# Kernel tuning notes

Measured on AMD Instinct MI355X. Metric: run time of the kernel, lower is better.

The kernel has to match this reference:

```python
import jax, jax.numpy as jnp
import numpy as np

N_STATE = 128      # HiPPO state size (hardcoded N=128 in module)
SEQ = 8192         # sequence length
D_HEAD = 16        # d_model=128 // n_head=8, used only for score scaling
OUT_DIM = 1000     # hardcoded self.out_dim
STEP = 1e-3        # step_size


def _legs_matrices(N):
    # HiPPO-LegS: A[n,k] = -sqrt(2n+1)sqrt(2k+1) (n>k), -(n+1) (n==k), 0 else; B[n]=sqrt(2n+1)
    n = np.arange(N, dtype=np.float64)
    pre = np.sqrt(2.0 * n + 1.0)
    A = -np.tril(pre[:, None] * pre[None, :], -1) - np.diag(n + 1.0)
    B = pre.copy()
    return A, B


def setup_inputs() -> dict:
    key = jax.random.key(0)
    kq, kk, kv, kw = jax.random.split(key, 4)
    A_np, B_np = _legs_matrices(N_STATE)
    A = jnp.asarray(A_np, jnp.float32)
    B = jnp.asarray(B_np, jnp.float32)
    # ZOH discretization (GBT_alpha=2.0 > 1 in repo => zero-order hold)
    GA = jax.scipy.linalg.expm(STEP * A)                       # (N, N)
    GB = jnp.linalg.solve(A, (GA - jnp.eye(N_STATE)) @ B)      # (N,)
    # xavier-uniform proj kernel (128 -> 1000), zero bias
    lim = float(np.sqrt(6.0 / (N_STATE + OUT_DIM)))
    Wp = jax.random.uniform(kw, (N_STATE, OUT_DIM), jnp.float32, -lim, lim)
    bp = jnp.zeros((OUT_DIM,), jnp.float32)
    return {
        "query": jax.random.normal(kq, (SEQ, 1), jnp.float32),
        "key": jax.random.normal(kk, (SEQ, 1), jnp.float32),
        "value": jax.random.normal(kv, (SEQ, 1), jnp.float32),
        "GA": GA,
        "GB": GB,
        "Wp": Wp,
        "bp": bp,
    }


def _hippo_scan(GA, GB, fs):
    # fs: (3, S) scalar input sequences; carry c: (3, N)
    def step(c, ft):
        c = c @ GA.T + ft[:, None] * GB[None, :]
        return c, c
    c0 = jnp.zeros((fs.shape[0], GA.shape[0]), GA.dtype)
    _, cs = jax.lax.scan(step, c0, fs.T)   # cs: (S, 3, N)
    return cs


def reference(query, key, value, GA, GB, Wp, bp):
    fs = jnp.stack([query[:, 0], key[:, 0], value[:, 0]])  # (3, S)
    cs = _hippo_scan(GA, GB, fs)                            # (S, 3, N)
    q, k, v = cs[:, 0, :], cs[:, 1, :], cs[:, 2, :]         # (S, N) each
    score = (q @ k.T) / jnp.sqrt(jnp.asarray(D_HEAD, q.dtype))  # (S, S)
    attn = jax.nn.softmax(score, axis=-1)
    context = attn @ v                                      # (S, N)
    out = context @ Wp + bp                                 # (S, OUT_DIM)
    return out, attn
```

## Files before the change

kernel.cpp:

```cpp
#include <hip/hip_runtime.h>

static constexpr int N  = 128;
static constexpr int S  = 8192;
static constexpr int L  = 128;
static constexpr int NC = 64;
static constexpr int OD = 1000;
static constexpr int KSPLIT = 16;
#define SCL 0.25f

typedef unsigned short u16;
typedef __attribute__((ext_vector_type(4))) unsigned short us4;
typedef __attribute__((ext_vector_type(8))) unsigned short us8;
typedef __attribute__((ext_vector_type(8))) short bf16x8;
typedef __attribute__((ext_vector_type(4))) float f32x4;

__device__ __forceinline__ u16 f2bf(float x){
  unsigned u = __float_as_uint(x);
  u += 0x7FFFu + ((u >> 16) & 1u);
  return (u16)(u >> 16);
}
__device__ __forceinline__ float bf2f(u16 h){
  return __uint_as_float(((unsigned)h) << 16);
}

__global__ void k_copyT(const float* __restrict__ GA, float* __restrict__ QT1){
  int idx = blockIdx.x*256 + threadIdx.x;
  int m = idx >> 7, n = idx & 127;
  QT1[idx] = GA[n*N + m];
}

__global__ __launch_bounds__(256) void k_powmm(float* QT, int mlev){
  int i = blockIdx.z + 1;
  const float* Am = QT + (size_t)mlev*(N*N);
  const float* Ai = QT + (size_t)i*(N*N);
  float* C = QT + (size_t)(mlev+i)*(N*N);
  __shared__ __align__(16) float As[16][68];
  __shared__ __align__(16) float Bs[16][68];
  int bm = blockIdx.y, bn = blockIdx.x;
  int tx = threadIdx.x, ty = threadIdx.y;
  int tid = ty*16 + tx;
  float acc[4][4] = {};
  for (int kt = 0; kt < N; kt += 16){
    int row = tid >> 2, kc = (tid & 3) << 2;
    float4 av = *(const float4*)(Am + (size_t)(bm*64+row)*N + kt + kc);
    As[kc+0][row]=av.x; As[kc+1][row]=av.y; As[kc+2][row]=av.z; As[kc+3][row]=av.w;
    int bk = tid >> 4, c0 = (tid & 15) << 2;
    *(float4*)&Bs[bk][c0] = *(const float4*)(Ai + (size_t)(kt+bk)*N + bn*64 + c0);
    __syncthreads();
#pragma unroll
    for (int kk = 0; kk < 16; ++kk){
      float4 a = *(const float4*)&As[kk][ty*4];
      float4 b = *(const float4*)&Bs[kk][tx*4];
      float aa[4]={a.x,a.y,a.z,a.w}, bb[4]={b.x,b.y,b.z,b.w};
#pragma unroll
      for (int ii=0; ii<4; ++ii)
#pragma unroll
        for (int jj=0; jj<4; ++jj) acc[ii][jj] += aa[ii]*bb[jj];
    }
    __syncthreads();
  }
#pragma unroll
  for (int ii=0; ii<4; ++ii){
    float4 vst = make_float4(acc[ii][0],acc[ii][1],acc[ii][2],acc[ii][3]);
    *(float4*)(C + (size_t)(bm*64+ty*4+ii)*N + bn*64 + tx*4) = vst;
  }
}

__global__ void k_g(const float* __restrict__ QT, const float* __restrict__ GB,
                    float* __restrict__ g){
  int kb = blockIdx.x;
  int n = threadIdx.x;
  if (kb == 0){ g[n] = GB[n]; return; }
  const float* Qk = QT + (size_t)kb*(N*N);
  float acc = 0.0f;
  for (int m = 0; m < N; ++m) acc += Qk[m*N + n]*GB[m];
  g[kb*N + n] = acc;
}

__global__ __launch_bounds__(256) void k_fill_local(const float* __restrict__ fq,
                             const float* __restrict__ fk, const float* __restrict__ fv,
                             const float* __restrict__ g, float* __restrict__ cs){
  int tile = blockIdx.x;
  int s = blockIdx.y, j = blockIdx.z;
  const float* f = (s==0)? fq : (s==1)? fk : fv;
  __shared__ float flp[256];
  __shared__ __align__(16) float Bs[16][68];
  int tx = threadIdx.x, ty = threadIdx.y;
  int tid = ty*16 + tx;
  flp[tid] = (tid < 128) ? 0.0f : f[j*L + tid - 128];
  int ti = tile >> 1, tj = tile & 1;
  float acc[4][4] = {};
  int kmax = (ti == 0) ? 64 : 128;
  for (int kt = 0; kt < kmax; kt += 16){
    int bk = tid >> 4, c0 = (tid & 15) << 2;
    *(float4*)&Bs[bk][c0] = *(const float4*)(g + (size_t)(kt+bk)*N + tj*64 + c0);
    __syncthreads();
#pragma unroll
    for (int kk = 0; kk < 16; ++kk){
      float4 b = *(const float4*)&Bs[kk][tx*4];
      int base = 128 + ti*64 + ty*4 - kt - kk;
      float aa[4] = {flp[base], flp[base+1], flp[base+2], flp[base+3]};
      float bb[4] = {b.x, b.y, b.z, b.w};
#pragma unroll
      for (int ii=0; ii<4; ++ii)
#pragma unroll
        for (int jj=0; jj<4; ++jj) acc[ii][jj] += aa[ii]*bb[jj];
    }
    __syncthreads();
  }
#pragma unroll
  for (int ii=0; ii<4; ++ii){
    int row = ti*64 + ty*4 + ii;
    float4 vst = make_float4(acc[ii][0],acc[ii][1],acc[ii][2],acc[ii][3]);
    *(float4*)(cs + ((size_t)s*S + (size_t)j*L + row)*N + tj*64 + tx*4) = vst;
  }
}

__global__ void k_bscan(const float* __restrict__ QT, const float* __restrict__ cs,
                        float* __restrict__ bounds){
  __shared__ float bc[3][N];
  __shared__ float bnx[3][N];
  int tid = threadIdx.x;
  int s = tid >> 7, n = tid & 127;
  const float* QL = QT + (size_t)L*(N*N);
  bc[s][n] = 0.0f;
  bounds[(0*3+s)*N + n] = 0.0f;
  __syncthreads();
  for (int j = 0; j < NC; ++j){
    float acc = cs[((size_t)s*S + (size_t)j*L + 127)*N + n];
    for (int m = 0; m < N; ++m) acc += QL[m*N+n]*bc[s][m];
    bnx[s][n] = acc;
    bounds[((j+1)*3+s)*N + n] = acc;
    __syncthreads();
    bc[s][n] = bnx[s][n];
    __syncthreads();
  }
}

__global__ __launch_bounds__(256) void k_fill_bound(const float* __restrict__ QT,
                          const float* __restrict__ bounds, float* __restrict__ cs){
  int i = blockIdx.x;
  int jg = blockIdx.y;
  __shared__ float Qs[N*N];
  int tid = threadIdx.x;
  int p = tid >> 7, n = tid & 127;
  const float* Qg = QT + (size_t)(i+1)*(N*N);
  for (int idx = tid; idx < N*N; idx += 256) Qs[idx] = Qg[idx];
  __syncthreads();
  for (int r4 = 0; r4 < 24; r4 += 4){
    int task0 = jg*48 + p*24 + r4;
    const float* b0 = bounds + (size_t)task0*N;
    const float* b1 = b0 + N;
    const float* b2 = b0 + 2*N;
    const float* b3 = b0 + 3*N;
    float a0=0.f, a1=0.f, a2=0.f, a3=0.f;
#pragma unroll 4
    for (int m = 0; m < N; ++m){
      float q = Qs[m*N + n];
      a0 += q*b0[m]; a1 += q*b1[m]; a2 += q*b2[m]; a3 += q*b3[m];
    }
    float av[4] = {a0, a1, a2, a3};
#pragma unroll
    for (int q4 = 0; q4 < 4; ++q4){
      int task = task0 + q4;
      int j = task/3, s2 = task - 3*j;
      cs[((size_t)s2*S + (size_t)j*L + i)*N + n] += av[q4];
    }
  }
}

__global__ void k_split_qk(const float* __restrict__ cs,
                           u16* __restrict__ sh, u16* __restrict__ sl){
  size_t i = ((size_t)blockIdx.x*256 + threadIdx.x) << 2;
  float4 v = *(const float4*)(cs + i);
  us4 h, l;
  h[0]=f2bf(v.x); l[0]=f2bf(v.x - bf2f(h[0]));
  h[1]=f2bf(v.y); l[1]=f2bf(v.y - bf2f(h[1]));
  h[2]=f2bf(v.z); l[2]=f2bf(v.z - bf2f(h[2]));
  h[3]=f2bf(v.w); l[3]=f2bf(v.w - bf2f(h[3]));
  *(us4*)(sh + i) = h;
  *(us4*)(sl + i) = l;
}

__global__ __launch_bounds__(256) void k_split_vT(const float* __restrict__ vs,
                           u16* __restrict__ vth, u16* __restrict__ vtl){
  __shared__ u16 Th[128*72];
  __shared__ u16 Tl[128*72];
  int t0 = blockIdx.x * 64;
  int tid = threadIdx.x;
  for (int c = tid; c < 2048; c += 256){
    int i = c >> 5, n0 = (c & 31) << 2;
    float4 v = *(const float4*)(vs + (size_t)(t0 + i)*N + n0);
    u16 h;
    h = f2bf(v.x); Th[(n0+0)*72 + i] = h; Tl[(n0+0)*72 + i] = f2bf(v.x - bf2f(h));
    h = f2bf(v.y); Th[(n0+1)*72 + i] = h; Tl[(n0+1)*72 + i] = f2bf(v.y - bf2f(h));
    h = f2bf(v.z); Th[(n0+2)*72 + i] = h; Tl[(n0+2)*72 + i] = f2bf(v.z - bf2f(h));
    h = f2bf(v.w); Th[(n0+3)*72 + i] = h; Tl[(n0+3)*72 + i] = f2bf(v.w - bf2f(h));
  }
  __syncthreads();
  for (int c = tid; c < 1024; c += 256){
    int n = c >> 3, tc = (c & 7) << 3;
    int tile = (t0 + tc) >> 5;
    int kin  = (t0 + tc) & 31;
    size_t dst = (size_t)tile*4096 + n*32 + kin;
    *(us8*)(vth + dst) = *(const us8*)&Th[n*72 + tc];
    *(us8*)(vtl + dst) = *(const us8*)&Tl[n*72 + tc];
  }
}

__global__ __launch_bounds__(256) void k_stats(
    const u16* __restrict__ qh, const u16* __restrict__ ql,
    const u16* __restrict__ kh, const u16* __restrict__ kl,
    float* __restrict__ pmax, float* __restrict__ psum){
  __shared__ __align__(16) u16 Ah[128*40], Al[128*40], Bh[128*40], Bl[128*40];
  __shared__ float wst[2][128][2];
  int bm = blockIdx.y, bn = blockIdx.x;
  int tid = threadIdx.x;
  int lane = tid & 63, w = tid >> 6;
  int l15 = lane & 15, l4 = lane >> 4;
  int wr = w >> 1, wc = w & 1;
  int kg = l4 << 3;
  f32x4 accs[4][4] = {};
  for (int kt = 0; kt < N; kt += 32){
    for (int c = tid; c < 512; c += 256){
      int r = c >> 2, k8 = (c & 3) << 3;
      size_t ga = (size_t)(bm*128 + r)*N + kt + k8;
      size_t gb = (size_t)(bn*128 + r)*N + kt + k8;
      int lo = r*40 + k8;
      *(us8*)&Ah[lo] = *(const us8*)(qh + ga);
      *(us8*)&Al[lo] = *(const us8*)(ql + ga);
      *(us8*)&Bh[lo] = *(const us8*)(kh + gb);
      *(us8*)&Bl[lo] = *(const us8*)(kl + gb);
    }
    __syncthreads();
    bf16x8 kfh[4], kfl[4], qfh[4], qfl[4];
#pragma unroll
    for (int si = 0; si < 4; ++si){
      kfh[si] = *(const bf16x8*)&Bh[(wr*64 + si*16 + l15)*40 + kg];
      kfl[si] = *(const bf16x8*)&Bl[(wr*64 + si*16 + l15)*40 + kg];
    }
#pragma unroll
    for (int qi = 0; qi < 4; ++qi){
      qfh[qi] = *(const bf16x8*)&Ah[(wc*64 + qi*16 + l15)*40 + kg];
      qfl[qi] = *(const bf16x8*)&Al[(wc*64 + qi*16 + l15)*40 + kg];
    }
#pragma unroll
    for (int si = 0; si < 4; ++si)
#pragma unroll
      for (int qi = 0; qi < 4; ++qi){
        accs[si][qi] = __builtin_amdgcn_mfma_f32_16x16x32_bf16(kfh[si], qfh[qi], accs[si][qi], 0,0,0);
        accs[si][qi] = __builtin_amdgcn_mfma_f32_16x16x32_bf16(kfh[si], qfl[qi], accs[si][qi], 0,0,0);
        accs[si][qi] = __builtin_amdgcn_mfma_f32_16x16x32_bf16(kfl[si], qfh[qi], accs[si][qi], 0,0,0);
      }
    __syncthreads();
  }
  float mq[4], sq[4];
#pragma unroll
  for (int qi = 0; qi < 4; ++qi){
    float m = -3.0e38f;
#pragma unroll
    for (int si = 0; si < 4; ++si)
#pragma unroll
      for (int r = 0; r < 4; ++r) m = fmaxf(m, accs[si][qi][r]);
    mq[qi] = m * SCL;
  }
#pragma unroll
  for (int qi = 0; qi < 4; ++qi){
    mq[qi] = fmaxf(mq[qi], __shfl_xor(mq[qi], 16, 64));
    mq[qi] = fmaxf(mq[qi], __shfl_xor(mq[qi], 32, 64));
  }
#pragma unroll
  for (int qi = 0; qi < 4; ++qi){
    float s = 0.0f;
#pragma unroll
    for (int si = 0; si < 4; ++si)
#pragma unroll
      for (int r = 0; r < 4; ++r) s += __expf(accs[si][qi][r]*SCL - mq[qi]);
    sq[qi] = s;
  }
#pragma unroll
  for (int qi = 0; qi < 4; ++qi){
    sq[qi] += __shfl_xor(sq[qi], 16, 64);
    sq[qi] += __shfl_xor(sq[qi], 32, 64);
  }
  if (l4 == 0){
#pragma unroll
    for (int qi = 0; qi < 4; ++qi){
      int ql_ = wc*64 + qi*16 + l15;
      wst[wr][ql_][0] = mq[qi];
      wst[wr][ql_][1] = sq[qi];
    }
  }
  __syncthreads();
  if (tid < 128){
    float m0 = wst[0][tid][0], m1 = wst[1][tid][0];
    float m = fmaxf(m0, m1);
    float Z = wst[0][tid][1]*__expf(m0 - m) + wst[1][tid][1]*__expf(m1 - m);
    pmax[(size_t)bn*S + bm*128 + tid] = m;
    psum[(size_t)bn*S + bm*128 + tid] = Z;
  }
}

__global__ void k_rowstat(const float* __restrict__ pmax, const float* __restrict__ psum,
                          float* __restrict__ rowm, float* __restrict__ rowinv){
  int t = blockIdx.x*256 + threadIdx.x;
  float m = -3.0e38f;
  for (int b = 0; b < 64; ++b) m = fmaxf(m, pmax[(size_t)b*S + t]);
  float Z = 0.0f;
  for (int b = 0; b < 64; ++b) Z += psum[(size_t)b*S + t]*__expf(pmax[(size_t)b*S + t] - m);
  rowm[t] = m;
  rowinv[t] = 1.0f/Z;
}

__global__ __launch_bounds__(256) void k_ctx(
    float* __restrict__ attn,
    const float* __restrict__ rowm, const float* __restrict__ rowinv,
    const u16* __restrict__ qh, const u16* __restrict__ ql,
    const u16* __restrict__ kh, const u16* __restrict__ kl,
    const u16* __restrict__ vth, const u16* __restrict__ vtl,
    float* __restrict__ dst, int mode){
  __shared__ __align__(16) u16 Ksh[32*136], Ksl[32*136];
  __shared__ __align__(16) u16 Vsh[128*40], Vsl[128*40];
  int bm = blockIdx.x, kz = blockIdx.y;
  int tid = threadIdx.x, lane = tid & 63, w = tid >> 6;
  int l15 = lane & 15, l4 = lane >> 4;
  int kg = l4 << 3;
  const int KC = S / KSPLIT;
  int k0 = kz*KC;
  int qrow0 = bm*128 + w*32;
  bf16x8 qfh[2][4], qfl[2][4];
  float rm[2], ri[2];
#pragma unroll
  for (int qi = 0; qi < 2; ++qi){
    int q = qrow0 + qi*16 + l15;
#pragma unroll
    for (int kt = 0; kt < 4; ++kt){
      qfh[qi][kt] = *(const bf16x8*)(qh + (size_t)q*N + kt*32 + kg);
      qfl[qi][kt] = *(const bf16x8*)(ql + (size_t)q*N + kt*32 + kg);
    }
    rm[qi] = rowm[q];
    ri[qi] = rowinv[q];
  }
  f32x4 acco[2][8] = {};
  for (int ko = 0; ko < KC/32; ++ko){
    int cb = k0 + ko*32;
    for (int c = tid; c < 512; c += 256){
      int rr = c >> 4, k8 = (c & 15) << 3;
      size_t gk = (size_t)(cb + rr)*N + k8;
      *(us8*)&Ksh[rr*136 + k8] = *(const us8*)(kh + gk);
      *(us8*)&Ksl[rr*136 + k8] = *(const us8*)(kl + gk);
    }
    {
      const u16* sh = vth + (size_t)(cb >> 5)*4096;
      const u16* sl = vtl + (size_t)(cb >> 5)*4096;
      for (int c = tid; c < 512; c += 256){
        int n = c >> 2, k8 = (c & 3) << 3;
        *(us8*)&Vsh[n*40 + k8] = *(const us8*)(sh + (size_t)c*8);
        *(us8*)&Vsl[n*40 + k8] = *(const us8*)(sl + (size_t)c*8);
      }
    }
    __syncthreads();
    f32x4 accs[2][2] = {};
#pragma unroll
    for (int kt = 0; kt < 4; ++kt){
      bf16x8 kfh[2], kfl[2];
#pragma unroll
      for (int si = 0; si < 2; ++si){
        kfh[si] = *(const bf16x8*)&Ksh[(si*16 + l15)*136 + kt*32 + kg];
        kfl[si] = *(const bf16x8*)&Ksl[(si*16 + l15)*136 + kt*32 + kg];
      }
#pragma unroll
      for (int si = 0; si < 2; ++si)
#pragma unroll
        for (int qi = 0; qi < 2; ++qi){
          accs[si][qi] = __builtin_amdgcn_mfma_f32_16x16x32_bf16(kfh[si], qfh[qi][kt], accs[si][qi], 0,0,0);
          accs[si][qi] = __builtin_amdgcn_mfma_f32_16x16x32_bf16(kfh[si], qfl[qi][kt], accs[si][qi], 0,0,0);
          accs[si][qi] = __builtin_amdgcn_mfma_f32_16x16x32_bf16(kfl[si], qfh[qi][kt], accs[si][qi], 0,0,0);
        }
    }
    bf16x8 pah[2][2], pal[2][2];
#pragma unroll
    for (int si = 0; si < 2; ++si)
#pragma unroll
      for (int qi = 0; qi < 2; ++qi){
        float p0 = __expf(accs[si][qi][0]*SCL - rm[qi]) * ri[qi];
        float p1 = __expf(accs[si][qi][1]*SCL - rm[qi]) * ri[qi];
        float p2 = __expf(accs[si][qi][2]*SCL - rm[qi]) * ri[qi];
        float p3 = __expf(accs[si][qi][3]*SCL - rm[qi]) * ri[qi];
        int q = qrow0 + qi*16 + l15;
        *(float4*)(attn + (size_t)q*S + cb + si*16 + (l4<<2)) = make_float4(p0,p1,p2,p3);
        u16 h0=f2bf(p0), h1=f2bf(p1), h2=f2bf(p2), h3=f2bf(p3);
        u16 e0=f2bf(p0-bf2f(h0)), e1=f2bf(p1-bf2f(h1)), e2=f2bf(p2-bf2f(h2)), e3=f2bf(p3-bf2f(h3));
        bf16x8 ah; ah[0]=(short)h0; ah[1]=(short)h1; ah[2]=(short)h2; ah[3]=(short)h3;
        ah[4]=0; ah[5]=0; ah[6]=0; ah[7]=0;
        bf16x8 al; al[0]=(short)e0; al[1]=(short)e1; al[2]=(short)e2; al[3]=(short)e3;
        al[4]=0; al[5]=0; al[6]=0; al[7]=0;
        pah[si][qi] = ah; pal[si][qi] = al;
      }
#pragma unroll
    for (int si = 0; si < 2; ++si)
#pragma unroll
      for (int ni = 0; ni < 8; ++ni){
        int vaddr = (ni*16 + l15)*40 + si*16 + (l4<<2);
        us4 vh4 = *(const us4*)&Vsh[vaddr];
        us4 vl4 = *(const us4*)&Vsl[vaddr];
        bf16x8 vh; vh[0]=(short)vh4[0]; vh[1]=(short)vh4[1]; vh[2]=(short)vh4[2]; vh[3]=(short)vh4[3];
        vh[4]=0; vh[5]=0; vh[6]=0; vh[7]=0;
        bf16x8 vl; vl[0]=(short)vl4[0]; vl[1]=(short)vl4[1]; vl[2]=(short)vl4[2]; vl[3]=(short)vl4[3];
        vl[4]=0; vl[5]=0; vl[6]=0; vl[7]=0;
#pragma unroll
        for (int qi = 0; qi < 2; ++qi){
          acco[qi][ni] = __builtin_amdgcn_mfma_f32_16x16x32_bf16(pah[si][qi], vh, acco[qi][ni], 0,0,0);
          acco[qi][ni] = __builtin_amdgcn_mfma_f32_16x16x32_bf16(pah[si][qi], vl, acco[qi][ni], 0,0,0);
          acco[qi][ni] = __builtin_amdgcn_mfma_f32_16x16x32_bf16(pal[si][qi], vh, acco[qi][ni], 0,0,0);
        }
      }
    __syncthreads();
  }
  if (mode == 0){
    float* P = dst + (size_t)kz*S*N;
#pragma unroll
    for (int qi = 0; qi < 2; ++qi)
#pragma unroll
      for (int ni = 0; ni < 8; ++ni)
#pragma unroll
        for (int r = 0; r < 4; ++r){
          int q = qrow0 + qi*16 + (l4<<2) + r;
          P[(size_t)q*N + ni*16 + l15] = acco[qi][ni][r];
        }
  } else {
#pragma unroll
    for (int qi = 0; qi < 2; ++qi)
#pragma unroll
      for (int ni = 0; ni < 8; ++ni)
#pragma unroll
        for (int r = 0; r < 4; ++r){
          int q = qrow0 + qi*16 + (l4<<2) + r;
          atomicAdd(&dst[(size_t)q*N + ni*16 + l15], acco[qi][ni][r]);
        }
  }
}

__global__ __launch_bounds__(256) void k_reduce(const float* __restrict__ part,
                                                float* __restrict__ ctx){
  size_t idx = (size_t)blockIdx.x*256 + threadIdx.x;
  const float4* p4 = (const float4*)part;
  float4 acc = p4[idx];
  const size_t stride = (size_t)S*N/4;
#pragma unroll
  for (int kz = 1; kz < KSPLIT; ++kz){
    float4 v = p4[(size_t)kz*stride + idx];
    acc.x += v.x; acc.y += v.y; acc.z += v.z; acc.w += v.w;
  }
  ((float4*)ctx)[idx] = acc;
}

__global__ __launch_bounds__(256) void k_out(const float* __restrict__ ctx,
                   const float* __restrict__ Wp, const float* __restrict__ bp,
                   float* __restrict__ out){
  __shared__ __align__(16) float As[16][68];
  __shared__ __align__(16) float Bs[16][68];
  int bn = blockIdx.x;
  int bm = blockIdx.y;
  int tx = threadIdx.x, ty = threadIdx.y;
  int tid = ty*16 + tx;
  float acc[4][4] = {};
  for (int kt = 0; kt < N; kt += 16){
    int row = tid >> 2, kc = (tid & 3) << 2;
    float4 av = *(const float4*)(ctx + (size_t)(bm*64+row)*N + kt + kc);
    As[kc+0][row]=av.x; As[kc+1][row]=av.y; As[kc+2][row]=av.z; As[kc+3][row]=av.w;
    int bk = tid >> 4, c0 = (tid & 15) << 2;
#pragma unroll
    for (int jj = 0; jj < 4; ++jj){
      int c = bn*64 + c0 + jj;
      Bs[bk][c0+jj] = (c < OD) ? Wp[(size_t)(kt+bk)*OD + c] : 0.0f;
    }
    __syncthreads();
#pragma unroll
    for (int kk = 0; kk < 16; ++kk){
      float4 a = *(const float4*)&As[kk][ty*4];
      float4 b = *(const float4*)&Bs[kk][tx*4];
      float aa[4]={a.x,a.y,a.z,a.w}, bb[4]={b.x,b.y,b.z,b.w};
#pragma unroll
      for (int ii=0; ii<4; ++ii)
#pragma unroll
        for (int jj=0; jj<4; ++jj) acc[ii][jj] += aa[ii]*bb[jj];
    }
    __syncthreads();
  }
#pragma unroll
  for (int ii=0; ii<4; ++ii){
    int r = bm*64 + ty*4 + ii;
#pragma unroll
    for (int jj=0; jj<4; ++jj){
      int c = bn*64 + tx*4 + jj;
      if (c < OD) out[(size_t)r*OD + c] = acc[ii][jj] + bp[c];
    }
  }
}

extern "C" void kernel_launch(void* const* d_in, const int* in_sizes, int n_in,
                              void* d_out, int out_size, void* d_ws, size_t ws_size,
                              hipStream_t stream){
  const float* fq = (const float*)d_in[0];
  const float* fk = (const float*)d_in[1];
  const float* fv = (const float*)d_in[2];
  const float* GA = (const float*)d_in[3];
  const float* GB = (const float*)d_in[4];
  const float* Wp = (const float*)d_in[5];
  const float* bp = (const float*)d_in[6];
  float* out  = (float*)d_out;
  float* attn = out + (size_t)S*OD;

  float* ws     = (float*)d_ws;
  float* QT     = ws;
  float* g      = QT + (size_t)129*N*N;
  float* bounds = g + (size_t)L*N;
  float* cs     = bounds + (size_t)(NC+1)*3*N;
  float* ctx    = cs + (size_t)3*S*N;
  u16*   qkh    = (u16*)(ctx + (size_t)S*N);
  u16*   qkl    = qkh + (size_t)2*S*N;
  u16*   vth    = qkl + (size_t)2*S*N;
  u16*   vtl    = vth + (size_t)S*N;
  float* pmax   = (float*)(vtl + (size_t)S*N);
  float* psum   = pmax + (size_t)(S/128)*S;
  float* rowm   = psum + (size_t)(S/128)*S;
  float* rowinv = rowm + S;
  float* part   = rowinv + S;
  size_t need_part = ((size_t)(part - ws) + (size_t)KSPLIT*S*N) * sizeof(float);
  bool use_part = (ws_size >= need_part);

  k_copyT<<<64, 256, 0, stream>>>(GA, QT + (size_t)N*N);
  for (int m = 1; m < L; m <<= 1)
    k_powmm<<<dim3(2,2,m), dim3(16,16), 0, stream>>>(QT, m);
  k_g<<<128, 128, 0, stream>>>(QT, GB, g);
  k_fill_local<<<dim3(4,3,NC), dim3(16,16), 0, stream>>>(fq, fk, fv, g, cs);
  k_bscan<<<1, 384, 0, stream>>>(QT, cs, bounds);
  k_fill_bound<<<dim3(L,4), 256, 0, stream>>>(QT, bounds, cs);

  k_split_qk<<<(2*S*N)/1024, 256, 0, stream>>>(cs, qkh, qkl);
  k_split_vT<<<S/64, 256, 0, stream>>>(cs + (size_t)2*S*N, vth, vtl);

  k_stats<<<dim3(S/128, S/128), 256, 0, stream>>>(
      qkh, qkl, qkh + (size_t)S*N, qkl + (size_t)S*N, pmax, psum);
  k_rowstat<<<S/256, 256, 0, stream>>>(pmax, psum, rowm, rowinv);
  if (use_part){
    k_ctx<<<dim3(S/128, KSPLIT), 256, 0, stream>>>(attn, rowm, rowinv,
        qkh, qkl, qkh + (size_t)S*N, qkl + (size_t)S*N, vth, vtl, part, 0);
    k_reduce<<<(S*N/4)/256, 256, 0, stream>>>(part, ctx);
  } else {
    hipMemsetAsync(ctx, 0, (size_t)S*N*sizeof(float), stream);
    k_ctx<<<dim3(S/128, KSPLIT), 256, 0, stream>>>(attn, rowm, rowinv,
        qkh, qkl, qkh + (size_t)S*N, qkl + (size_t)S*N, vth, vtl, ctx, 1);
  }
  k_out<<<dim3(16, S/64), dim3(16,16), 0, stream>>>(ctx, Wp, bp, out);
}
```

Before: 896.8 us.

## Halve PV MFMA count by shuffling scores into full K=32 operands

The score tiles are redistributed across lanes with cross-lane shuffles, so each lane holds eight contiguous probabilities. The P·V product can then use full 32-wide MFMA operands instead of half-zero-padded ones, which halves the PV MFMA count. The K tile in shared memory also switches from padded rows to an XOR-swizzled layout. Q fragments are now reloaded from global memory inside each chunk rather than kept in registers, which lowers register pressure but adds repeated global and L1 traffic.

```diff
diff --git a/kernel.cpp b/kernel.cpp
--- a/kernel.cpp
+++ b/kernel.cpp
@@ -319,7 +319,7 @@
     const u16* __restrict__ kh, const u16* __restrict__ kl,
     const u16* __restrict__ vth, const u16* __restrict__ vtl,
     float* __restrict__ dst, int mode){
-  __shared__ __align__(16) u16 Ksh[32*136], Ksl[32*136];
+  __shared__ __align__(16) u16 Ksh[32*128], Ksl[32*128];
   __shared__ __align__(16) u16 Vsh[128*40], Vsl[128*40];
   int bm = blockIdx.x, kz = blockIdx.y;
   int tid = threadIdx.x, lane = tid & 63, w = tid >> 6;
@@ -327,94 +327,98 @@
   int kg = l4 << 3;
   const int KC = S / KSPLIT;
   int k0 = kz*KC;
-  int qrow0 = bm*128 + w*32;
-  bf16x8 qfh[2][4], qfl[2][4];
+  int qbase = bm*128 + w*32;
   float rm[2], ri[2];
-#pragma unroll
-  for (int qi = 0; qi < 2; ++qi){
-    int q = qrow0 + qi*16 + l15;
-#pragma unroll
-    for (int kt = 0; kt < 4; ++kt){
-      qfh[qi][kt] = *(const bf16x8*)(qh + (size_t)q*N + kt*32 + kg);
-      qfl[qi][kt] = *(const bf16x8*)(ql + (size_t)q*N + kt*32 + kg);
-    }
-    rm[qi] = rowm[q];
-    ri[qi] = rowinv[q];
-  }
+  rm[0] = rowm[qbase + l15];        ri[0] = rowinv[qbase + l15];
+  rm[1] = rowm[qbase + 16 + l15];   ri[1] = rowinv[qbase + 16 + l15];
+  int src0 = l15 + 32*(l4 & 1);
+  int src1 = src0 + 16;
+  bool hi_si = (l4 >> 1);
   f32x4 acco[2][8] = {};
-  for (int ko = 0; ko < KC/32; ++ko){
-    int cb = k0 + ko*32;
+  for (int ko = 0; ko < KC; ko += 32){
+    int cb = k0 + ko;
     for (int c = tid; c < 512; c += 256){
-      int rr = c >> 4, k8 = (c & 15) << 3;
-      size_t gk = (size_t)(cb + rr)*N + k8;
-      *(us8*)&Ksh[rr*136 + k8] = *(const us8*)(kh + gk);
-      *(us8*)&Ksl[rr*136 + k8] = *(const us8*)(kl + gk);
+      int rr = c >> 4, c8 = (c & 15) << 3;
+      int lo = (rr*128 + c8) ^ ((rr & 7) << 3);
+      size_t gk = (size_t)(cb + rr)*N + c8;
+      *(us8*)&Ksh[lo] = *(const us8*)(kh + gk);
+      *(us8*)&Ksl[lo] = *(const us8*)(kl + gk);
     }
     {
       const u16* sh = vth + (size_t)(cb >> 5)*4096;
       const u16* sl = vtl + (size_t)(cb >> 5)*4096;
       for (int c = tid; c < 512; c += 256){
-        int n = c >> 2, k8 = (c & 3) << 3;
-        *(us8*)&Vsh[n*40 + k8] = *(const us8*)(sh + (size_t)c*8);
-        *(us8*)&Vsl[n*40 + k8] = *(const us8*)(sl + (size_t)c*8);
+        int lo = (c >> 2)*40 + ((c & 3) << 3);
+        *(us8*)&Vsh[lo] = *(const us8*)(sh + (size_t)c*8);
+        *(us8*)&Vsl[lo] = *(const us8*)(sl + (size_t)c*8);
       }
     }
     __syncthreads();
     f32x4 accs[2][2] = {};
 #pragma unroll
     for (int kt = 0; kt < 4; ++kt){
-      bf16x8 kfh[2], kfl[2];
+      bf16x8 qfh[2], qfl[2], kfh[2], kfl[2];
+#pragma unroll
+      for (int qi = 0; qi < 2; ++qi){
+        size_t gq = (size_t)(qbase + qi*16 + l15)*N + kt*32 + kg;
+        qfh[qi] = *(const bf16x8*)(qh + gq);
+        qfl[qi] = *(const bf16x8*)(ql + gq);
+      }
 #pragma unroll
       for (int si = 0; si < 2; ++si){
-        kfh[si] = *(const bf16x8*)&Ksh[(si*16 + l15)*136 + kt*32 + kg];
-        kfl[si] = *(const bf16x8*)&Ksl[(si*16 + l15)*136 + kt*32 + kg];
+        int lo = (((si*16 + l15)*128 + kt*32 + kg) ^ (((si*16 + l15) & 7) << 3));
+        kfh[si] = *(const bf16x8*)&Ksh[lo];
+        kfl[si] = *(const bf16x8*)&Ksl[lo];
       }
 #pragma unroll
       for (int si = 0; si < 2; ++si)
 #pragma unroll
         for (int qi = 0; qi < 2; ++qi){
-          accs[si][qi] = __builtin_amdgcn_mfma_f32_16x16x32_bf16(kfh[si], qfh[qi][kt], accs[si][qi], 0,0,0);
-          accs[si][qi] = __builtin_amdgcn_mfma_f32_16x16x32_bf16(kfh[si], qfl[qi][kt], accs[si][qi], 0,0,0);
-          accs[si][qi] = __builtin_amdgcn_mfma_f32_16x16x32_bf16(kfl[si], qfh[qi][kt], accs[si][qi], 0,0,0);
+          accs[si][qi] = __builtin_amdgcn_mfma_f32_16x16x32_bf16(kfh[si], qfh[qi], accs[si][qi], 0,0,0);
+          accs[si][qi] = __builtin_amdgcn_mfma_f32_16x16x32_bf16(kfh[si], qfl[qi], accs[si][qi], 0,0,0);
+          accs[si][qi] = __builtin_amdgcn_mfma_f32_16x16x32_bf16(kfl[si], qfh[qi], accs[si][qi], 0,0,0);
         }
     }
-    bf16x8 pah[2][2], pal[2][2];
-#pragma unroll
-    for (int si = 0; si < 2; ++si)
+    bf16x8 pah[2], pal[2];
+#pragma unroll
+    for (int qi = 0; qi < 2; ++qi){
+      float y[8];
+#pragma unroll
+      for (int r = 0; r < 4; ++r){
+        float t0 = __shfl(accs[0][qi][r], src0, 64);
+        float t1 = __shfl(accs[1][qi][r], src0, 64);
+        y[r] = hi_si ? t1 : t0;
+        float u0 = __shfl(accs[0][qi][r], src1, 64);
+        float u1 = __shfl(accs[1][qi][r], src1, 64);
+        y[4+r] = hi_si ? u1 : u0;
+      }
+      float p[8];
+#pragma unroll
+      for (int j = 0; j < 8; ++j) p[j] = __expf(y[j]*SCL - rm[qi]) * ri[qi];
+      int q = qbase + qi*16 + l15;
+      *(float4*)(attn + (size_t)q*S + cb + kg)     = make_float4(p[0],p[1],p[2],p[3]);
+      *(float4*)(attn + (size_t)q*S + cb + kg + 4) = make_float4(p[4],p[5],p[6],p[7]);
+      bf16x8 ah, al;
+#pragma unroll
+      for (int j = 0; j < 8; ++j){
+        u16 h = f2bf(p[j]);
+        ah[j] = (short)h;
+        al[j] = (short)f2bf(p[j] - bf2f(h));
+      }
+      pah[qi] = ah; pal[qi] = al;
+    }
+#pragma unroll
+    for (int ni = 0; ni < 8; ++ni){
+      int lo = (ni*16 + l15)*40 + kg;
+      bf16x8 vbh = *(const bf16x8*)&Vsh[lo];
+      bf16x8 vbl = *(const bf16x8*)&Vsl[lo];
 #pragma unroll
       for (int qi = 0; qi < 2; ++qi){
-        float p0 = __expf(accs[si][qi][0]*SCL - rm[qi]) * ri[qi];
-        float p1 = __expf(accs[si][qi][1]*SCL - rm[qi]) * ri[qi];
-        float p2 = __expf(accs[si][qi][2]*SCL - rm[qi]) * ri[qi];
-        float p3 = __expf(accs[si][qi][3]*SCL - rm[qi]) * ri[qi];
-        int q = qrow0 + qi*16 + l15;
-        *(float4*)(attn + (size_t)q*S + cb + si*16 + (l4<<2)) = make_float4(p0,p1,p2,p3);
-        u16 h0=f2bf(p0), h1=f2bf(p1), h2=f2bf(p2), h3=f2bf(p3);
-        u16 e0=f2bf(p0-bf2f(h0)), e1=f2bf(p1-bf2f(h1)), e2=f2bf(p2-bf2f(h2)), e3=f2bf(p3-bf2f(h3));
-        bf16x8 ah; ah[0]=(short)h0; ah[1]=(short)h1; ah[2]=(short)h2; ah[3]=(short)h3;
-        ah[4]=0; ah[5]=0; ah[6]=0; ah[7]=0;
-        bf16x8 al; al[0]=(short)e0; al[1]=(short)e1; al[2]=(short)e2; al[3]=(short)e3;
-        al[4]=0; al[5]=0; al[6]=0; al[7]=0;
-        pah[si][qi] = ah; pal[si][qi] = al;
-      }
-#pragma unroll
-    for (int si = 0; si < 2; ++si)
-#pragma unroll
-      for (int ni = 0; ni < 8; ++ni){
-        int vaddr = (ni*16 + l15)*40 + si*16 + (l4<<2);
-        us4 vh4 = *(const us4*)&Vsh[vaddr];
-        us4 vl4 = *(const us4*)&Vsl[vaddr];
-        bf16x8 vh; vh[0]=(short)vh4[0]; vh[1]=(short)vh4[1]; vh[2]=(short)vh4[2]; vh[3]=(short)vh4[3];
-        vh[4]=0; vh[5]=0; vh[6]=0; vh[7]=0;
-        bf16x8 vl; vl[0]=(short)vl4[0]; vl[1]=(short)vl4[1]; vl[2]=(short)vl4[2]; vl[3]=(short)vl4[3];
-        vl[4]=0; vl[5]=0; vl[6]=0; vl[7]=0;
-#pragma unroll
-        for (int qi = 0; qi < 2; ++qi){
-          acco[qi][ni] = __builtin_amdgcn_mfma_f32_16x16x32_bf16(pah[si][qi], vh, acco[qi][ni], 0,0,0);
-          acco[qi][ni] = __builtin_amdgcn_mfma_f32_16x16x32_bf16(pah[si][qi], vl, acco[qi][ni], 0,0,0);
-          acco[qi][ni] = __builtin_amdgcn_mfma_f32_16x16x32_bf16(pal[si][qi], vh, acco[qi][ni], 0,0,0);
-        }
-      }
+        acco[qi][ni] = __builtin_amdgcn_mfma_f32_16x16x32_bf16(pah[qi], vbh, acco[qi][ni], 0,0,0);
+        acco[qi][ni] = __builtin_amdgcn_mfma_f32_16x16x32_bf16(pah[qi], vbl, acco[qi][ni], 0,0,0);
+        acco[qi][ni] = __builtin_amdgcn_mfma_f32_16x16x32_bf16(pal[qi], vbh, acco[qi][ni], 0,0,0);
+      }
+    }
     __syncthreads();
   }
   if (mode == 0){
@@ -425,7 +429,7 @@
       for (int ni = 0; ni < 8; ++ni)
 #pragma unroll
         for (int r = 0; r < 4; ++r){
-          int q = qrow0 + qi*16 + (l4<<2) + r;
+          int q = qbase + qi*16 + (l4<<2) + r;
           P[(size_t)q*N + ni*16 + l15] = acco[qi][ni][r];
         }
   } else {
@@ -435,7 +439,7 @@
       for (int ni = 0; ni < 8; ++ni)
 #pragma unroll
         for (int r = 0; r < 4; ++r){
-          int q = qrow0 + qi*16 + (l4<<2) + r;
+          int q = qbase + qi*16 + (l4<<2) + r;
           atomicAdd(&dst[(size_t)q*N + ni*16 + l15], acco[qi][ni][r]);
         }
   }
```

New measurement: 895.7 us. About the same (-0.1%).
